# Performance work log

Measured on AMD Instinct MI355X. Metric: run time of the kernel, lower is better.

The kernel has to match this reference:

```python
import jax, jax.numpy as jnp
import numpy as np

EPS = 1e-5  # nn.RMSNorm eps


def setup_inputs() -> dict:
    key = jax.random.key(0)
    ks = jax.random.split(key, 8)
    B, L, D, R = 4, 4096, 2048, 4
    return {
        "h": jax.random.normal(ks[0], (B, L, D), jnp.float32),
        "h_o": jax.random.normal(ks[1], (B, L, D), jnp.float32),
        "static_alpha": jax.random.normal(ks[2], (R, R + 1), jnp.float32),
        "static_beta": jax.random.normal(ks[3], (R,), jnp.float32),
        "dynamic_alpha_fn": jax.random.normal(ks[4], (D, R + 1), jnp.float32) * 0.02,
        "dynamic_alpha_scale": jax.random.uniform(ks[5], (1,), jnp.float32, 0.005, 0.02),
        "dynamic_beta_fn": jax.random.normal(ks[6], (D,), jnp.float32) * 0.02,
        "dynamic_beta_scale": jnp.array([0.01], jnp.float32),
        "rms_weight": jax.random.uniform(ks[7], (D,), jnp.float32, 0.5, 1.5),
    }


def reference(h, h_o, static_alpha, static_beta, dynamic_alpha_fn,
              dynamic_alpha_scale, dynamic_beta_fn, dynamic_beta_scale,
              rms_weight):
    # RMSNorm over last dim with learnable weight (dynamic branch only)
    h_norm = h * jax.lax.rsqrt(jnp.mean(h * h, axis=-1, keepdims=True) + EPS) * rms_weight

    # dynamic alpha: [B,L,rate+1] offset broadcast against static [rate,rate+1]
    alpha_offset = jnp.tanh(h_norm @ dynamic_alpha_fn) * dynamic_alpha_scale  # [B,L,R+1]
    alpha = alpha_offset[:, :, None, :] + static_alpha                        # [B,L,R,R+1]

    # dynamic beta: scalar offset per token broadcast against static [rate]
    beta_offset = jnp.tanh(h_norm @ dynamic_beta_fn) * dynamic_beta_scale     # [B,L] * [1]
    beta = beta_offset[..., None] + static_beta                               # [B,L,R]

    # connect_width: mix_h[b,l,c,d] = sum_r alpha[b,l,r,c] * h[b,l,d]
    mix_h = jnp.einsum('blrc,bld->blcd', alpha, h)                            # [B,L,R+1,D]

    # connect_depth: broadcast outer product beta x h_o plus old streams, sum over rate
    out = jnp.sum(beta[..., None] * h_o[:, :, None, :] + mix_h[:, :, 1:, :], axis=2)
    return out  # [B,L,D]
```

## Files before the change

kernel.cpp:

```cpp
#include <hip/hip_runtime.h>
#include <math.h>


constexpr int D    = 2048;
constexpr int RATE = 4;
constexpr float EPS = 1e-5f;
constexpr int TPB  = 8;
constexpr int NT   = 512;

__device__ __forceinline__ float fast_tanh(float x) {
    const float e = __expf(2.0f * x);
    return 1.0f - 2.0f / (e + 1.0f);
}

template<int CTRL>
__device__ __forceinline__ float dpp_add(float x) {
    int m = __builtin_amdgcn_update_dpp(0, __float_as_int(x), CTRL, 0xf, 0xf, true);
    return x + __int_as_float(m);
}

__device__ __forceinline__ float wave_sum_lane63(float x) {
    x = dpp_add<0x111>(x);
    x = dpp_add<0x112>(x);
    x = dpp_add<0x114>(x);
    x = dpp_add<0x118>(x);
    x = dpp_add<0x142>(x);
    x = dpp_add<0x143>(x);
    return x;
}

__global__ __launch_bounds__(NT, 4) void hyperconn_kernel(
    const float* __restrict__ h,
    const float* __restrict__ h_o,
    const float* __restrict__ sa,
    const float* __restrict__ sb,
    const float* __restrict__ fa,
    const float* __restrict__ a_sc,
    const float* __restrict__ fb,
    const float* __restrict__ b_sc,
    const float* __restrict__ w,
    float* __restrict__ out)
{
    const int tid  = threadIdx.x;
    const int d0   = tid * 4;
    const int wave = tid >> 6;
    const size_t t0 = (size_t)blockIdx.x * TPB;

    float4 hA[TPB];
    #pragma unroll
    for (int i = 0; i < TPB; ++i)
        hA[i] = *reinterpret_cast<const float4*>(h + (t0 + i) * D + d0);

    const float4 wq  = *reinterpret_cast<const float4*>(w + d0);
    const float wv[4] = {wq.x, wq.y, wq.z, wq.w};
    float fav[16];
    {
        float tmp[20];
        #pragma unroll
        for (int q = 0; q < 5; ++q) {
            float4 t = *reinterpret_cast<const float4*>(fa + (size_t)d0 * 5 + q * 4);
            tmp[q*4+0]=t.x; tmp[q*4+1]=t.y; tmp[q*4+2]=t.z; tmp[q*4+3]=t.w;
        }
        #pragma unroll
        for (int j = 0; j < 4; ++j)
            #pragma unroll
            for (int c = 0; c < 4; ++c)
                fav[j*4+c] = tmp[j*5 + 1 + c];
    }
    const float4 fbq = *reinterpret_cast<const float4*>(fb + d0);
    const float fbv[4] = {fbq.x, fbq.y, fbq.z, fbq.w};

    const float a4 = a_sc[0] * (float)RATE;
    const float b4 = b_sc[0] * (float)RATE;
    float cs = 0.f;
    #pragma unroll
    for (int r = 0; r < RATE; ++r)
        #pragma unroll
        for (int c = 1; c <= RATE; ++c)
            cs += sa[r * (RATE + 1) + c];
    const float sbsum = sb[0] + sb[1] + sb[2] + sb[3];

    __shared__ float  red[TPB][48];
    __shared__ float2 s2[TPB];

    #pragma unroll
    for (int i = 0; i < TPB; ++i) {
        const float hv[4] = {hA[i].x, hA[i].y, hA[i].z, hA[i].w};
        float acc[6] = {0.f, 0.f, 0.f, 0.f, 0.f, 0.f};
        #pragma unroll
        for (int j = 0; j < 4; ++j) {
            const float x  = hv[j];
            const float xw = x * wv[j];
            acc[0] = fmaf(x,  x,          acc[0]);
            acc[1] = fmaf(xw, fav[j*4+0], acc[1]);
            acc[2] = fmaf(xw, fav[j*4+1], acc[2]);
            acc[3] = fmaf(xw, fav[j*4+2], acc[3]);
            acc[4] = fmaf(xw, fav[j*4+3], acc[4]);
            acc[5] = fmaf(xw, fbv[j],     acc[5]);
        }
        #pragma unroll
        for (int k = 0; k < 6; ++k) acc[k] = wave_sum_lane63(acc[k]);
        if ((tid & 63) == 63) {
            #pragma unroll
            for (int k = 0; k < 6; ++k) red[i][wave * 6 + k] = acc[k];
        }
    }

    __syncthreads();

    if (tid < TPB) {
        float tot[6] = {0.f, 0.f, 0.f, 0.f, 0.f, 0.f};
        #pragma unroll
        for (int v = 0; v < 8; ++v)
            #pragma unroll
            for (int k = 0; k < 6; ++k)
                tot[k] += red[tid][v * 6 + k];
        const float rms  = rsqrtf(tot[0] * (1.0f / (float)D) + EPS);
        const float s_h  = a4 * (fast_tanh(tot[1] * rms) + fast_tanh(tot[2] * rms) +
                                 fast_tanh(tot[3] * rms) + fast_tanh(tot[4] * rms)) + cs;
        const float s_ho = b4 * fast_tanh(tot[5] * rms) + sbsum;
        s2[tid] = make_float2(s_h, s_ho);
    }

    __syncthreads();

    #pragma unroll
    for (int i = 0; i < TPB; ++i) {
        const float2 s = s2[i];
        const size_t base = (t0 + i) * D + d0;
        const float4 oq = *reinterpret_cast<const float4*>(h_o + base);
        float4 r;
        r.x = fmaf(s.y, oq.x, s.x * hA[i].x);
        r.y = fmaf(s.y, oq.y, s.x * hA[i].y);
        r.z = fmaf(s.y, oq.z, s.x * hA[i].z);
        r.w = fmaf(s.y, oq.w, s.x * hA[i].w);
        *reinterpret_cast<float4*>(out + base) = r;
    }
}

extern "C" void kernel_launch(void* const* d_in, const int* in_sizes, int n_in,
                              void* d_out, int out_size, void* d_ws, size_t ws_size,
                              hipStream_t stream) {
    const float* h    = (const float*)d_in[0];
    const float* h_o  = (const float*)d_in[1];
    const float* sa   = (const float*)d_in[2];
    const float* sb   = (const float*)d_in[3];
    const float* fa   = (const float*)d_in[4];
    const float* a_sc = (const float*)d_in[5];
    const float* fb   = (const float*)d_in[6];
    const float* b_sc = (const float*)d_in[7];
    const float* w    = (const float*)d_in[8];
    float* out = (float*)d_out;

    const int ntok   = in_sizes[0] / D;
    const int blocks = ntok / TPB;
    hyperconn_kernel<<<blocks, NT, 0, stream>>>(h, h_o, sa, sb, fa, a_sc, fb, b_sc, w, out);
}
```

Measured before the change: 79.68 us.

## Prefetch h_o before reduction and parallelize per-token finalize across waves

Loads all h_o rows into registers up front alongside h, so the second stream's memory latency overlaps the reduction instead of following the barrier. The per-token finalize is now done by each wave for its own token instead of by eight threads of one wave, and __syncthreads is replaced by an explicit LDS wait plus barrier. The occupancy hint in launch_bounds is removed. This raises register pressure (two 8-token float4 arrays per thread), which can lower occupancy.

Measured after the change: 80.46 us. No clear change (+1.0%).

```diff
diff --git a/kernel.cpp b/kernel.cpp
--- a/kernel.cpp
+++ b/kernel.cpp
@@ -29,7 +29,13 @@
     return x;
 }
 
-__global__ __launch_bounds__(NT, 4) void hyperconn_kernel(
+__device__ __forceinline__ void lds_barrier() {
+    asm volatile("s_waitcnt lgkmcnt(0)" ::: "memory");
+    __builtin_amdgcn_s_barrier();
+    __builtin_amdgcn_sched_barrier(0);
+}
+
+__global__ __launch_bounds__(NT) void hyperconn_kernel(
     const float* __restrict__ h,
     const float* __restrict__ h_o,
     const float* __restrict__ sa,
@@ -44,31 +50,35 @@
     const int tid  = threadIdx.x;
     const int d0   = tid * 4;
     const int wave = tid >> 6;
+    const int lane = tid & 63;
     const size_t t0 = (size_t)blockIdx.x * TPB;
 
-    float4 hA[TPB];
+    const float4 wq  = *reinterpret_cast<const float4*>(w + d0);
+    float tmp[20];
+    #pragma unroll
+    for (int q = 0; q < 5; ++q) {
+        float4 t = *reinterpret_cast<const float4*>(fa + (size_t)d0 * 5 + q * 4);
+        tmp[q*4+0]=t.x; tmp[q*4+1]=t.y; tmp[q*4+2]=t.z; tmp[q*4+3]=t.w;
+    }
+    const float4 fbq = *reinterpret_cast<const float4*>(fb + d0);
+
+    float4 hA[TPB], oA[TPB];
     #pragma unroll
     for (int i = 0; i < TPB; ++i)
         hA[i] = *reinterpret_cast<const float4*>(h + (t0 + i) * D + d0);
+    #pragma unroll
+    for (int i = 0; i < TPB; ++i)
+        oA[i] = *reinterpret_cast<const float4*>(h_o + (t0 + i) * D + d0);
+    asm volatile("" ::: "memory");
 
-    const float4 wq  = *reinterpret_cast<const float4*>(w + d0);
-    const float wv[4] = {wq.x, wq.y, wq.z, wq.w};
+    const float wv[4]  = {wq.x, wq.y, wq.z, wq.w};
+    const float fbv[4] = {fbq.x, fbq.y, fbq.z, fbq.w};
     float fav[16];
-    {
-        float tmp[20];
+    #pragma unroll
+    for (int j = 0; j < 4; ++j)
         #pragma unroll
-        for (int q = 0; q < 5; ++q) {
-            float4 t = *reinterpret_cast<const float4*>(fa + (size_t)d0 * 5 + q * 4);
-            tmp[q*4+0]=t.x; tmp[q*4+1]=t.y; tmp[q*4+2]=t.z; tmp[q*4+3]=t.w;
-        }
-        #pragma unroll
-        for (int j = 0; j < 4; ++j)
-            #pragma unroll
-            for (int c = 0; c < 4; ++c)
-                fav[j*4+c] = tmp[j*5 + 1 + c];
-    }
-    const float4 fbq = *reinterpret_cast<const float4*>(fb + d0);
-    const float fbv[4] = {fbq.x, fbq.y, fbq.z, fbq.w};
+        for (int c = 0; c < 4; ++c)
+            fav[j*4+c] = tmp[j*5 + 1 + c];
 
     const float a4 = a_sc[0] * (float)RATE;
     const float b4 = b_sc[0] * (float)RATE;
@@ -100,40 +110,40 @@
         }
         #pragma unroll
         for (int k = 0; k < 6; ++k) acc[k] = wave_sum_lane63(acc[k]);
-        if ((tid & 63) == 63) {
+        if (lane == 63) {
             #pragma unroll
             for (int k = 0; k < 6; ++k) red[i][wave * 6 + k] = acc[k];
         }
     }
 
-    __syncthreads();
+    lds_barrier();
 
-    if (tid < TPB) {
+    {
+        const int i = wave;
         float tot[6] = {0.f, 0.f, 0.f, 0.f, 0.f, 0.f};
         #pragma unroll
         for (int v = 0; v < 8; ++v)
             #pragma unroll
             for (int k = 0; k < 6; ++k)
-                tot[k] += red[tid][v * 6 + k];
+                tot[k] += red[i][v * 6 + k];
         const float rms  = rsqrtf(tot[0] * (1.0f / (float)D) + EPS);
         const float s_h  = a4 * (fast_tanh(tot[1] * rms) + fast_tanh(tot[2] * rms) +
                                  fast_tanh(tot[3] * rms) + fast_tanh(tot[4] * rms)) + cs;
         const float s_ho = b4 * fast_tanh(tot[5] * rms) + sbsum;
-        s2[tid] = make_float2(s_h, s_ho);
+        if (lane == 0) s2[i] = make_float2(s_h, s_ho);
     }
 
-    __syncthreads();
+    lds_barrier();
 
     #pragma unroll
     for (int i = 0; i < TPB; ++i) {
         const float2 s = s2[i];
         const size_t base = (t0 + i) * D + d0;
-        const float4 oq = *reinterpret_cast<const float4*>(h_o + base);
         float4 r;
-        r.x = fmaf(s.y, oq.x, s.x * hA[i].x);
-        r.y = fmaf(s.y, oq.y, s.x * hA[i].y);
-        r.z = fmaf(s.y, oq.z, s.x * hA[i].z);
-        r.w = fmaf(s.y, oq.w, s.x * hA[i].w);
+        r.x = fmaf(s.y, oA[i].x, s.x * hA[i].x);
+        r.y = fmaf(s.y, oA[i].y, s.x * hA[i].y);
+        r.z = fmaf(s.y, oA[i].z, s.x * hA[i].z);
+        r.w = fmaf(s.y, oA[i].w, s.x * hA[i].w);
         *reinterpret_cast<float4*>(out + base) = r;
     }
 }
```
